# Performance work log

Measured on AMD Instinct MI355X. Metric: run time of the kernel, lower is better.

Reference implementation:

```python
import jax, jax.numpy as jnp
import numpy as np

B, T, H, W, C = 2, 4, 128, 128, 192
HEADS = 6
WS = 8          # attention window (per-frame, wsD=1)
OW = 12         # overlapping KV window: 8 + int(8*0.5)
PAD = (OW - WS) // 2
TBL = (WS + OW - 1) ** 2   # 361 relative-position-bias entries
MLP_HID = C * 2


def setup_inputs() -> dict:
    key = jax.random.key(0)
    ks = jax.random.split(key, 8)
    s = 0.02
    return dict(
        x=jax.random.normal(ks[0], (B, T, H, W, C), jnp.float32),
        x_size=jnp.array([H, W], jnp.int32),  # unused by forward (shadowed), kept for signature fidelity
        rpi_oca=jax.random.randint(ks[1], (WS * WS, OW * OW), 0, TBL),
        norm1_g=jnp.ones((C,), jnp.float32), norm1_b=jnp.zeros((C,), jnp.float32),
        qkv_w=jax.random.normal(ks[2], (C, 3 * C), jnp.float32) * s,
        qkv_b=jnp.zeros((3 * C,), jnp.float32),
        rpb_table=jax.random.normal(ks[3], (TBL, HEADS), jnp.float32) * s,
        norm2_g=jnp.ones((C,), jnp.float32), norm2_b=jnp.zeros((C,), jnp.float32),
        fc1_w=jax.random.normal(ks[4], (C, MLP_HID), jnp.float32) * s,
        fc1_b=jnp.zeros((MLP_HID,), jnp.float32),
        fc2_w=jax.random.normal(ks[5], (MLP_HID, C), jnp.float32) * s,
        fc2_b=jnp.zeros((C,), jnp.float32),
    )


def _ln(x, g, b):
    m = x.mean(-1, keepdims=True)
    v = ((x - m) ** 2).mean(-1, keepdims=True)
    return (x - m) * jax.lax.rsqrt(v + 1e-5) * g + b


def reference(x, x_size, rpi_oca, norm1_g, norm1_b, qkv_w, qkv_b, rpb_table,
              norm2_g, norm2_b, fc1_w, fc1_b, fc2_w, fc2_b):
    b, t, h, w, c = x.shape
    d = c // HEADS
    scale = d ** -0.5
    nH, nW = h // WS, w // WS
    b_ = b * t * nH * nW  # total windows
    shortcut = x
    xn = _ln(x, norm1_g, norm1_b)
    qkv = (xn @ qkv_w + qkv_b).reshape(b, t, h, w, 3, c)
    q, k, v = qkv[..., 0, :], qkv[..., 1, :], qkv[..., 2, :]
    # --- query: non-overlapping (1,8,8) windows -> (b_, heads, 64, d)
    qw = (q.reshape(b, t, nH, WS, nW, WS, c)
           .transpose(0, 1, 2, 4, 3, 5, 6)
           .reshape(b_, WS * WS, HEADS, d)
           .transpose(0, 2, 1, 3))
    # --- key/value: overlapping (1,12,12) windows with stride 8, zero-padded by 2
    hid = (jnp.arange(nH) * WS)[:, None] + jnp.arange(OW)  # (nH, OW)
    wid = (jnp.arange(nW) * WS)[:, None] + jnp.arange(OW)  # (nW, OW)

    def owin(z):
        zp = jnp.pad(z, ((0, 0), (0, 0), (PAD, PAD), (PAD, PAD), (0, 0)))
        zw = zp[:, :, hid][:, :, :, :, wid]  # (b, t, nH, OW, nW, OW, c)
        return (zw.transpose(0, 1, 2, 4, 3, 5, 6)
                  .reshape(b_, OW * OW, HEADS, d)
                  .transpose(0, 2, 1, 3))

    kw, vw = owin(k), owin(v)
    attn = jnp.einsum('bhqd,bhkd->bhqk', qw * scale, kw)  # (b_, heads, 64, 144)
    bias = rpb_table[rpi_oca.reshape(-1)].reshape(WS * WS, OW * OW, HEADS).transpose(2, 0, 1)
    attn = attn + bias[None]  # NOTE: original forward applies NO softmax (self.softmax unused)
    out = (jnp.einsum('bhqk,bhkd->bhqd', attn, vw)
             .transpose(0, 2, 1, 3)
             .reshape(b_, WS * WS, c))
    # window_reverse
    xa = (out.reshape(b, t, nH, nW, WS, WS, c)
             .transpose(0, 1, 2, 4, 3, 5, 6)
             .reshape(b, t, h, w, c))
    x = xa + shortcut  # self.proj is never applied in the original forward
    hmlp = jax.nn.gelu(_ln(x, norm2_g, norm2_b) @ fc1_w + fc1_b, approximate=False)
    return x + (hmlp @ fc2_w + fc2_b)
```

## Files before the change

### kernel.cpp

```cpp
#include <hip/hip_runtime.h>
#include <cstdint>
#include <cstddef>

typedef short bf16x8 __attribute__((ext_vector_type(8)));
typedef unsigned short u16x4 __attribute__((ext_vector_type(4)));
typedef float f32x4  __attribute__((ext_vector_type(4)));
typedef unsigned short u16;

#define DEVI __device__ __forceinline__

constexpr int C     = 192;
constexpr int HEADS = 6;
constexpr int NQKV  = 576;
constexpr int HID   = 384;
constexpr int NTOK  = 131072;

DEVI u16 f2bf(float f){
  union { float f; unsigned u; } v; v.f = f;
  return (u16)((v.u + 0x7fffu + ((v.u >> 16) & 1u)) >> 16);
}

DEVI float gelu(float xx){
  float y  = xx * 0.70710678118654752f;
  float ay = fabsf(y);
  float t  = __builtin_amdgcn_rcpf(1.0f + 0.3275911f * ay);
  float p  = t*(0.254829592f + t*(-0.284496736f + t*(1.421413741f + t*(-1.453152027f + t*1.061405429f))));
  float e  = __expf(-(y*y));
  float er = copysignf(1.0f - p*e, y);
  return 0.5f * xx * (1.0f + er);
}

__global__ void prep_kernel(const float* __restrict__ qkv_w,
                            const float* __restrict__ fc1_w,
                            const float* __restrict__ fc2_w,
                            const int*   __restrict__ rpi,
                            const float* __restrict__ rpb,
                            u16* __restrict__ qkvP,
                            u16* __restrict__ fc1P,
                            u16* __restrict__ fc2P,
                            float* __restrict__ bias_pk){
  int idx = blockIdx.x * blockDim.x + threadIdx.x;
  int stride = gridDim.x * blockDim.x;
  for(int i = idx; i < 36*6*64*8; i += stride){
    int e = i & 7, lane = (i >> 3) & 63, t = i >> 9;
    int ks = t % 6, p = t / 6;
    int n = p*16 + (lane & 15), k = ks*32 + (lane >> 4)*8 + e;
    qkvP[i] = f2bf(qkv_w[k*NQKV + n]);
  }
  for(int i = idx; i < 24*6*64*8; i += stride){
    int e = i & 7, lane = (i >> 3) & 63, t = i >> 9;
    int ks = t % 6, p = t / 6;
    int n = p*16 + (lane & 15), k = ks*32 + (lane >> 4)*8 + e;
    fc1P[i] = f2bf(fc1_w[k*HID + n]);
  }
  for(int i = idx; i < 12*12*64*8; i += stride){
    int e = i & 7, lane = (i >> 3) & 63, t = i >> 9;
    int ks = t % 12, p = t / 12;
    int n = p*16 + (lane & 15), k = ks*32 + (lane >> 4)*8 + e;
    fc2P[i] = f2bf(fc2_w[k*C + n]);
  }
  const int n4 = HEADS*5*2*4*64*4;
  for(int i = idx; i < n4; i += stride){
    int t = i;
    int r    = t & 3;  t >>= 2;
    int lane = t & 63; t >>= 6;
    int mi   = t & 3;  t >>= 2;
    int nf   = t & 1;  t >>= 1;
    int chunk = t % 5; int head = t / 5;
    int q  = mi*16 + (lane & 15);
    int kk = chunk*32 + nf*16 + ((lane >> 4) << 2) + r;
    float v = 0.f;
    if(kk < 144) v = rpb[rpi[q*144 + kk]*HEADS + head];
    bias_pk[i] = v;
  }
}

__global__ __launch_bounds__(384, 4)
void qkv_kernel(const float* __restrict__ x,
                const float* __restrict__ g1,
                const float* __restrict__ b1,
                const u16* __restrict__ wP,
                const float* __restrict__ qb,
                u16* __restrict__ qkv){
  __shared__ u16 xn[64][200];
  __shared__ u16 rp[64][152];
  const int tid = threadIdx.x;
  const int bid = blockIdx.x;
  const int nh = (bid >> 3) & 1;
  const int tb = (bid & 7) + ((bid >> 4) << 3);
  const size_t tok0 = (size_t)tb * 64;
  if(tid < 256){
    const int trow = tid >> 2;
    const int j = tid & 3;
    const float* xr = x + (tok0 + trow)*C;
    float4 xv[12];
    #pragma unroll
    for(int u = 0; u < 12; ++u)
      xv[u] = *reinterpret_cast<const float4*>(xr + u*16 + j*4);
    float s1 = 0.f, s2 = 0.f;
    #pragma unroll
    for(int u = 0; u < 12; ++u){
      const float* f = reinterpret_cast<const float*>(&xv[u]);
      #pragma unroll
      for(int e = 0; e < 4; ++e){ s1 += f[e]; s2 += f[e]*f[e]; }
    }
    s1 += __shfl_xor(s1, 1, 64); s2 += __shfl_xor(s2, 1, 64);
    s1 += __shfl_xor(s1, 2, 64); s2 += __shfl_xor(s2, 2, 64);
    const float mean = s1 * (1.f/192.f);
    const float rstd = rsqrtf(s2*(1.f/192.f) - mean*mean + 1e-5f);
    #pragma unroll
    for(int u = 0; u < 12; ++u){
      const float4 gv = *reinterpret_cast<const float4*>(g1 + u*16 + j*4);
      const float4 bv = *reinterpret_cast<const float4*>(b1 + u*16 + j*4);
      const float* f = reinterpret_cast<const float*>(&xv[u]);
      const float* gp = reinterpret_cast<const float*>(&gv);
      const float* bp = reinterpret_cast<const float*>(&bv);
      u16x4 pk;
      #pragma unroll
      for(int e = 0; e < 4; ++e) pk[e] = f2bf((f[e] - mean)*rstd*gp[e] + bp[e]);
      *reinterpret_cast<u16x4*>(&xn[trow][u*16 + j*4]) = pk;
    }
  }
  __syncthreads();
  const int lane = tid & 63;
  const int wn = tid >> 6;
  const int g = lane >> 4, col = lane & 15;
  const f32x4 fzero = {0.f, 0.f, 0.f, 0.f};
  f32x4 acc[4][3];
  #pragma unroll
  for(int mi = 0; mi < 4; ++mi)
    #pragma unroll
    for(int nf = 0; nf < 3; ++nf) acc[mi][nf] = fzero;
  const int p0 = nh*18 + wn*3;
  #pragma unroll
  for(int ks = 0; ks < 6; ++ks){
    bf16x8 wf[3];
    #pragma unroll
    for(int nf = 0; nf < 3; ++nf)
      wf[nf] = *reinterpret_cast<const bf16x8*>(wP + ((size_t)(((p0 + nf)*6 + ks)*64) + lane)*8);
    bf16x8 a[4];
    #pragma unroll
    for(int mi = 0; mi < 4; ++mi)
      a[mi] = *reinterpret_cast<const bf16x8*>(&xn[mi*16 + col][ks*32 + g*8]);
    #pragma unroll
    for(int nf = 0; nf < 3; ++nf)
      #pragma unroll
      for(int mi = 0; mi < 4; ++mi)
        acc[mi][nf] = __builtin_amdgcn_mfma_f32_16x16x32_bf16(a[mi], wf[nf], acc[mi][nf], 0, 0, 0);
  }
  #pragma unroll
  for(int ph = 0; ph < 2; ++ph){
    if(wn >= ph*3 && wn < ph*3 + 3){
      const int wl = wn - ph*3;
      #pragma unroll
      for(int mi = 0; mi < 4; ++mi){
        #pragma unroll
        for(int nf = 0; nf < 3; ++nf){
          const int nloc = wl*48 + nf*16 + col;
          const float bb = qb[nh*288 + ph*144 + nloc];
          #pragma unroll
          for(int r = 0; r < 4; ++r)
            rp[mi*16 + g*4 + r][nloc] = f2bf(acc[mi][nf][r] + bb);
        }
      }
    }
    __syncthreads();
    #pragma unroll
    for(int it = 0; it < 3; ++it){
      const int c = tid + it*384;
      const int tok = c / 18, cc = c - tok*18;
      const int n0 = nh*288 + ph*144 + cc*8;
      const int pl = n0 >> 5, d0 = n0 & 31;
      bf16x8 vv = *reinterpret_cast<const bf16x8*>(&rp[tok][cc*8]);
      *reinterpret_cast<bf16x8*>(qkv + ((size_t)pl*NTOK + tok0 + tok)*32 + d0) = vv;
    }
    __syncthreads();
  }
}

__global__ __launch_bounds__(64, 2)
void attn_kernel(const u16* __restrict__ qkv,
                 const float* __restrict__ bias_pk,
                 const float* __restrict__ x,
                 float* __restrict__ out){
  __shared__ u16 Vt[32][168];
  __shared__ u16 Pl[64][40];
  const int lane = threadIdx.x;
  const int g = lane >> 4, col = lane & 15;
  const int win = blockIdx.x, head = blockIdx.y;
  const int bt = win >> 8, wh = (win >> 4) & 15, ww = win & 15;
  const int h0 = wh*8, w0 = ww*8;
  const size_t tokbase = (size_t)bt * 16384;
  const u16* Qp = qkv + (size_t)head      *NTOK*32;
  const u16* Kp = qkv + (size_t)(6 + head)*NTOK*32;
  const u16* Vp = qkv + (size_t)(12 + head)*NTOK*32;
  const bf16x8 z8 = {0,0,0,0,0,0,0,0};

  bf16x8 kf[10], vf[10];
  #pragma unroll
  for(int i = 0; i < 10; ++i){
    const int kr = i*16 + col;
    const int r12 = (kr*2731) >> 15;
    const int c12 = kr - r12*12;
    const int hh = h0 - 2 + r12;
    const int wp = w0 - 2 + c12;
    const bool valid = (kr < 144) && (hh >= 0) && (hh < 128) && (wp >= 0) && (wp < 128);
    const size_t t = valid ? (tokbase + (size_t)hh*128 + wp) : tokbase;
    bf16x8 kv_ = *reinterpret_cast<const bf16x8*>(Kp + t*32 + g*8);
    bf16x8 vv_ = *reinterpret_cast<const bf16x8*>(Vp + t*32 + g*8);
    kf[i] = valid ? kv_ : z8;
    vf[i] = valid ? vv_ : z8;
  }
  bf16x8 qf[4];
  #pragma unroll
  for(int mi = 0; mi < 4; ++mi){
    const int row = mi*16 + col;
    const size_t t = tokbase + (size_t)(h0 + (row >> 3))*128 + (w0 + (row & 7));
    qf[mi] = *reinterpret_cast<const bf16x8*>(Qp + t*32 + g*8);
  }
  #pragma unroll
  for(int i = 0; i < 10; ++i) asm volatile("" : "+v"(kf[i]));
  #pragma unroll
  for(int mi = 0; mi < 4; ++mi) asm volatile("" : "+v"(qf[mi]));
  #pragma unroll
  for(int i = 0; i < 10; ++i){
    const int kr = i*16 + col;
    #pragma unroll
    for(int e = 0; e < 8; ++e) Vt[g*8 + e][kr] = (u16)vf[i][e];
  }

  const f32x4 fzero = {0.f, 0.f, 0.f, 0.f};
  f32x4 oacc[4][2];
  #pragma unroll
  for(int mi = 0; mi < 4; ++mi){ oacc[mi][0] = fzero; oacc[mi][1] = fzero; }
  const float scale = 0.17677669529663689f;

  #pragma unroll
  for(int ch = 0; ch < 5; ++ch){
    float4 bv[2][4];
    #pragma unroll
    for(int nf = 0; nf < 2; ++nf)
      #pragma unroll
      for(int mi = 0; mi < 4; ++mi)
        bv[nf][mi] = *reinterpret_cast<const float4*>(
            bias_pk + (size_t)((((head*5 + ch)*2 + nf)*4 + mi)*64 + lane)*4);
    f32x4 st[2][4];
    #pragma unroll
    for(int nf = 0; nf < 2; ++nf)
      #pragma unroll
      for(int mi = 0; mi < 4; ++mi)
        st[nf][mi] = __builtin_amdgcn_mfma_f32_16x16x32_bf16(kf[ch*2 + nf], qf[mi], fzero, 0, 0, 0);
    #pragma unroll
    for(int nf = 0; nf < 2; ++nf){
      #pragma unroll
      for(int mi = 0; mi < 4; ++mi){
        const float* bp = reinterpret_cast<const float*>(&bv[nf][mi]);
        const float p0 = fmaf(st[nf][mi][0], scale, bp[0]);
        const float p1 = fmaf(st[nf][mi][1], scale, bp[1]);
        const float p2 = fmaf(st[nf][mi][2], scale, bp[2]);
        const float p3 = fmaf(st[nf][mi][3], scale, bp[3]);
        uint2 pw;
        pw.x = (unsigned)f2bf(p0) | ((unsigned)f2bf(p1) << 16);
        pw.y = (unsigned)f2bf(p2) | ((unsigned)f2bf(p3) << 16);
        *reinterpret_cast<uint2*>(
            reinterpret_cast<char*>(&Pl[0][0]) + (mi*16 + col)*80 + nf*32 + g*8) = pw;
      }
    }
    bf16x8 pa[4];
    #pragma unroll
    for(int mi = 0; mi < 4; ++mi)
      pa[mi] = *reinterpret_cast<const bf16x8*>(
          reinterpret_cast<const char*>(&Pl[0][0]) + (mi*16 + col)*80 + g*16);
    bf16x8 vfr[2];
    #pragma unroll
    for(int nf = 0; nf < 2; ++nf)
      vfr[nf] = *reinterpret_cast<const bf16x8*>(&Vt[nf*16 + col][ch*32 + g*8]);
    #pragma unroll
    for(int nf = 0; nf < 2; ++nf)
      #pragma unroll
      for(int mi = 0; mi < 4; ++mi)
        oacc[mi][nf] = __builtin_amdgcn_mfma_f32_16x16x32_bf16(pa[mi], vfr[nf], oacc[mi][nf], 0, 0, 0);
  }
  #pragma unroll
  for(int mi = 0; mi < 4; ++mi){
    #pragma unroll
    for(int nf = 0; nf < 2; ++nf){
      #pragma unroll
      for(int r = 0; r < 4; ++r){
        const int row = mi*16 + g*4 + r;
        const int hh = h0 + (row >> 3), wp = w0 + (row & 7);
        const size_t o = (tokbase + hh*128 + wp)*(size_t)C + head*32 + nf*16 + col;
        out[o] = oacc[mi][nf][r] + x[o];
      }
    }
  }
}

__global__ __launch_bounds__(512, 4)
void mlp_kernel(float* __restrict__ io,
                const float* __restrict__ g2,
                const float* __restrict__ b2,
                const u16* __restrict__ w1P,
                const float* __restrict__ fb1,
                const u16* __restrict__ w2P,
                const float* __restrict__ fb2){
  __shared__ u16 xn[64][200];
  __shared__ u16 hl[64][200];
  const int tid = threadIdx.x;
  const size_t tok0 = (size_t)blockIdx.x * 64;
  {
    const int trow = tid >> 3;
    const int j = tid & 7;
    const float* xr = io + (tok0 + trow)*C;
    float4 xv[6];
    #pragma unroll
    for(int u = 0; u < 6; ++u)
      xv[u] = *reinterpret_cast<const float4*>(xr + u*32 + j*4);
    float s1 = 0.f, s2 = 0.f;
    #pragma unroll
    for(int u = 0; u < 6; ++u){
      const float* f = reinterpret_cast<const float*>(&xv[u]);
      #pragma unroll
      for(int e = 0; e < 4; ++e){ s1 += f[e]; s2 += f[e]*f[e]; }
    }
    s1 += __shfl_xor(s1, 1, 64); s2 += __shfl_xor(s2, 1, 64);
    s1 += __shfl_xor(s1, 2, 64); s2 += __shfl_xor(s2, 2, 64);
    s1 += __shfl_xor(s1, 4, 64); s2 += __shfl_xor(s2, 4, 64);
    const float mean = s1 * (1.f/192.f);
    const float rstd = rsqrtf(s2*(1.f/192.f) - mean*mean + 1e-5f);
    #pragma unroll
    for(int u = 0; u < 6; ++u){
      const float4 gv = *reinterpret_cast<const float4*>(g2 + u*32 + j*4);
      const float4 bv = *reinterpret_cast<const float4*>(b2 + u*32 + j*4);
      const float* f = reinterpret_cast<const float*>(&xv[u]);
      const float* gp = reinterpret_cast<const float*>(&gv);
      const float* bp = reinterpret_cast<const float*>(&bv);
      u16x4 pk;
      #pragma unroll
      for(int e = 0; e < 4; ++e) pk[e] = f2bf((f[e] - mean)*rstd*gp[e] + bp[e]);
      *reinterpret_cast<u16x4*>(&xn[trow][u*32 + j*4]) = pk;
    }
  }
  __syncthreads();
  const int lane = tid & 63, wave = tid >> 6;
  const int wm = wave >> 2;
  const int wn = wave & 3;
  const int g = lane >> 4, col = lane & 15;
  const f32x4 fzero = {0.f, 0.f, 0.f, 0.f};
  f32x4 acc2[2][3];
  #pragma unroll
  for(int mi = 0; mi < 2; ++mi)
    #pragma unroll
    for(int nf = 0; nf < 3; ++nf) acc2[mi][nf] = fzero;
  #pragma unroll
  for(int hb = 0; hb < 2; ++hb){
    f32x4 acc1[2][3];
    #pragma unroll
    for(int mi = 0; mi < 2; ++mi)
      #pragma unroll
      for(int nf = 0; nf < 3; ++nf) acc1[mi][nf] = fzero;
    #pragma unroll
    for(int ks = 0; ks < 6; ++ks){
      bf16x8 wf[3];
      #pragma unroll
      for(int nf = 0; nf < 3; ++nf)
        wf[nf] = *reinterpret_cast<const bf16x8*>(w1P + ((size_t)(((hb*12 + wn*3 + nf)*6 + ks)*64) + lane)*8);
      bf16x8 a[2];
      #pragma unroll
      for(int mi = 0; mi < 2; ++mi)
        a[mi] = *reinterpret_cast<const bf16x8*>(&xn[wm*32 + mi*16 + col][ks*32 + g*8]);
      #pragma unroll
      for(int nf = 0; nf < 3; ++nf)
        #pragma unroll
        for(int mi = 0; mi < 2; ++mi)
          acc1[mi][nf] = __builtin_amdgcn_mfma_f32_16x16x32_bf16(a[mi], wf[nf], acc1[mi][nf], 0, 0, 0);
    }
    #pragma unroll
    for(int mi = 0; mi < 2; ++mi){
      #pragma unroll
      for(int nf = 0; nf < 3; ++nf){
        const int nl = wn*48 + nf*16 + col;
        const float bb = fb1[hb*192 + nl];
        #pragma unroll
        for(int r = 0; r < 4; ++r){
          const int row = wm*32 + mi*16 + g*4 + r;
          hl[row][nl] = f2bf(gelu(acc1[mi][nf][r] + bb));
        }
      }
    }
    __syncthreads();
    #pragma unroll
    for(int ks = 0; ks < 6; ++ks){
      bf16x8 wf[3];
      #pragma unroll
      for(int nf = 0; nf < 3; ++nf)
        wf[nf] = *reinterpret_cast<const bf16x8*>(w2P + ((size_t)(((wn*3 + nf)*12 + hb*6 + ks)*64) + lane)*8);
      bf16x8 a[2];
      #pragma unroll
      for(int mi = 0; mi < 2; ++mi)
        a[mi] = *reinterpret_cast<const bf16x8*>(&hl[wm*32 + mi*16 + col][ks*32 + g*8]);
      #pragma unroll
      for(int nf = 0; nf < 3; ++nf)
        #pragma unroll
        for(int mi = 0; mi < 2; ++mi)
          acc2[mi][nf] = __builtin_amdgcn_mfma_f32_16x16x32_bf16(a[mi], wf[nf], acc2[mi][nf], 0, 0, 0);
    }
    __syncthreads();
  }
  #pragma unroll
  for(int mi = 0; mi < 2; ++mi){
    #pragma unroll
    for(int nf = 0; nf < 3; ++nf){
      const int n = wn*48 + nf*16 + col;
      const float bb = fb2[n];
      #pragma unroll
      for(int r = 0; r < 4; ++r){
        const int row = wm*32 + mi*16 + g*4 + r;
        const size_t idx = (tok0 + row)*C + n;
        io[idx] = acc2[mi][nf][r] + bb + io[idx];
      }
    }
  }
}

extern "C" void kernel_launch(void* const* d_in, const int* in_sizes, int n_in,
                              void* d_out, int out_size, void* d_ws, size_t ws_size,
                              hipStream_t stream){
  const float* x    = (const float*)d_in[0];
  const int*   rpi  = (const int*)  d_in[2];
  const float* n1g  = (const float*)d_in[3];
  const float* n1b  = (const float*)d_in[4];
  const float* qkvw = (const float*)d_in[5];
  const float* qkvb = (const float*)d_in[6];
  const float* rpb  = (const float*)d_in[7];
  const float* n2g  = (const float*)d_in[8];
  const float* n2b  = (const float*)d_in[9];
  const float* fc1w = (const float*)d_in[10];
  const float* fc1b = (const float*)d_in[11];
  const float* fc2w = (const float*)d_in[12];
  const float* fc2b = (const float*)d_in[13];
  float* out = (float*)d_out;
  char* ws = (char*)d_ws;
  u16*   qkvP    = (u16*)  (ws + 0);
  u16*   fc1P    = (u16*)  (ws + 221184);
  u16*   fc2P    = (u16*)  (ws + 368640);
  float* bias_pk = (float*)(ws + 516096);
  u16*   qkvbuf  = (u16*)  (ws + 1499136);
  if(ws_size < 152494080ull) return;
  prep_kernel<<<dim3(512), dim3(256), 0, stream>>>(qkvw, fc1w, fc2w, rpi, rpb, qkvP, fc1P, fc2P, bias_pk);
  qkv_kernel<<<dim3(4096), dim3(384), 0, stream>>>(x, n1g, n1b, qkvP, qkvb, qkvbuf);
  attn_kernel<<<dim3(2048, 6), dim3(64), 0, stream>>>(qkvbuf, bias_pk, x, out);
  mlp_kernel<<<dim3(2048), dim3(512), 0, stream>>>(out, n2g, n2b, fc1P, fc1b, fc2P, fc2b);
}
```

Baseline: 280.8 us.

## Split attention window across four waves sharing K/V through LDS

```diff
diff --git a/kernel.cpp b/kernel.cpp
--- a/kernel.cpp
+++ b/kernel.cpp
@@ -178,14 +178,17 @@
   }
 }
 
-__global__ __launch_bounds__(64, 2)
+__global__ __launch_bounds__(256, 4)
 void attn_kernel(const u16* __restrict__ qkv,
                  const float* __restrict__ bias_pk,
                  const float* __restrict__ x,
                  float* __restrict__ out){
+  __shared__ u16 Kl[160][40];
   __shared__ u16 Vt[32][168];
   __shared__ u16 Pl[64][40];
-  const int lane = threadIdx.x;
+  const int tid  = threadIdx.x;
+  const int lane = tid & 63;
+  const int w    = tid >> 6;
   const int g = lane >> 4, col = lane & 15;
   const int win = blockIdx.x, head = blockIdx.y;
   const int bt = win >> 8, wh = (win >> 4) & 15, ww = win & 15;
@@ -196,107 +199,90 @@
   const u16* Vp = qkv + (size_t)(12 + head)*NTOK*32;
   const bf16x8 z8 = {0,0,0,0,0,0,0,0};
 
-  bf16x8 kf[10], vf[10];
-  #pragma unroll
-  for(int i = 0; i < 10; ++i){
-    const int kr = i*16 + col;
-    const int r12 = (kr*2731) >> 15;
-    const int c12 = kr - r12*12;
-    const int hh = h0 - 2 + r12;
-    const int wp = w0 - 2 + c12;
-    const bool valid = (kr < 144) && (hh >= 0) && (hh < 128) && (wp >= 0) && (wp < 128);
-    const size_t t = valid ? (tokbase + (size_t)hh*128 + wp) : tokbase;
-    bf16x8 kv_ = *reinterpret_cast<const bf16x8*>(Kp + t*32 + g*8);
-    bf16x8 vv_ = *reinterpret_cast<const bf16x8*>(Vp + t*32 + g*8);
-    kf[i] = valid ? kv_ : z8;
-    vf[i] = valid ? vv_ : z8;
-  }
-  bf16x8 qf[4];
-  #pragma unroll
-  for(int mi = 0; mi < 4; ++mi){
-    const int row = mi*16 + col;
+  #pragma unroll
+  for(int ii = 0; ii < 3; ++ii){
+    const int i = w + ii*4;
+    if(i < 10){
+      const int kr = i*16 + col;
+      const int r12 = (kr*2731) >> 15;
+      const int c12 = kr - r12*12;
+      const int hh = h0 - 2 + r12;
+      const int wp = w0 - 2 + c12;
+      const bool valid = (kr < 144) && (hh >= 0) && (hh < 128) && (wp >= 0) && (wp < 128);
+      const size_t t = valid ? (tokbase + (size_t)hh*128 + wp) : tokbase;
+      bf16x8 kv_ = *reinterpret_cast<const bf16x8*>(Kp + t*32 + g*8);
+      bf16x8 vv_ = *reinterpret_cast<const bf16x8*>(Vp + t*32 + g*8);
+      kv_ = valid ? kv_ : z8;
+      vv_ = valid ? vv_ : z8;
+      *reinterpret_cast<bf16x8*>(&Kl[kr][g*8]) = kv_;
+      #pragma unroll
+      for(int e = 0; e < 8; ++e) Vt[g*8 + e][kr] = (u16)vv_[e];
+    }
+  }
+  bf16x8 qf;
+  {
+    const int row = w*16 + col;
     const size_t t = tokbase + (size_t)(h0 + (row >> 3))*128 + (w0 + (row & 7));
-    qf[mi] = *reinterpret_cast<const bf16x8*>(Qp + t*32 + g*8);
-  }
-  #pragma unroll
-  for(int i = 0; i < 10; ++i) asm volatile("" : "+v"(kf[i]));
-  #pragma unroll
-  for(int mi = 0; mi < 4; ++mi) asm volatile("" : "+v"(qf[mi]));
-  #pragma unroll
-  for(int i = 0; i < 10; ++i){
-    const int kr = i*16 + col;
-    #pragma unroll
-    for(int e = 0; e < 8; ++e) Vt[g*8 + e][kr] = (u16)vf[i][e];
-  }
+    qf = *reinterpret_cast<const bf16x8*>(Qp + t*32 + g*8);
+  }
+  __syncthreads();
 
   const f32x4 fzero = {0.f, 0.f, 0.f, 0.f};
-  f32x4 oacc[4][2];
-  #pragma unroll
-  for(int mi = 0; mi < 4; ++mi){ oacc[mi][0] = fzero; oacc[mi][1] = fzero; }
+  f32x4 oacc[2];
+  oacc[0] = fzero; oacc[1] = fzero;
   const float scale = 0.17677669529663689f;
 
   #pragma unroll
   for(int ch = 0; ch < 5; ++ch){
-    float4 bv[2][4];
+    float4 bv[2];
     #pragma unroll
     for(int nf = 0; nf < 2; ++nf)
-      #pragma unroll
-      for(int mi = 0; mi < 4; ++mi)
-        bv[nf][mi] = *reinterpret_cast<const float4*>(
-            bias_pk + (size_t)((((head*5 + ch)*2 + nf)*4 + mi)*64 + lane)*4);
-    f32x4 st[2][4];
+      bv[nf] = *reinterpret_cast<const float4*>(
+          bias_pk + (size_t)((((head*5 + ch)*2 + nf)*4 + w)*64 + lane)*4);
+    bf16x8 kfr[2];
     #pragma unroll
     for(int nf = 0; nf < 2; ++nf)
-      #pragma unroll
-      for(int mi = 0; mi < 4; ++mi)
-        st[nf][mi] = __builtin_amdgcn_mfma_f32_16x16x32_bf16(kf[ch*2 + nf], qf[mi], fzero, 0, 0, 0);
+      kfr[nf] = *reinterpret_cast<const bf16x8*>(&Kl[ch*32 + nf*16 + col][g*8]);
+    f32x4 st[2];
+    #pragma unroll
+    for(int nf = 0; nf < 2; ++nf)
+      st[nf] = __builtin_amdgcn_mfma_f32_16x16x32_bf16(kfr[nf], qf, fzero, 0, 0, 0);
     #pragma unroll
     for(int nf = 0; nf < 2; ++nf){
-      #pragma unroll
-      for(int mi = 0; mi < 4; ++mi){
-        const float* bp = reinterpret_cast<const float*>(&bv[nf][mi]);
-        const float p0 = fmaf(st[nf][mi][0], scale, bp[0]);
-        const float p1 = fmaf(st[nf][mi][1], scale, bp[1]);
-        const float p2 = fmaf(st[nf][mi][2], scale, bp[2]);
-        const float p3 = fmaf(st[nf][mi][3], scale, bp[3]);
-        uint2 pw;
-        pw.x = (unsigned)f2bf(p0) | ((unsigned)f2bf(p1) << 16);
-        pw.y = (unsigned)f2bf(p2) | ((unsigned)f2bf(p3) << 16);
-        *reinterpret_cast<uint2*>(
-            reinterpret_cast<char*>(&Pl[0][0]) + (mi*16 + col)*80 + nf*32 + g*8) = pw;
-      }
-    }
-    bf16x8 pa[4];
-    #pragma unroll
-    for(int mi = 0; mi < 4; ++mi)
-      pa[mi] = *reinterpret_cast<const bf16x8*>(
-          reinterpret_cast<const char*>(&Pl[0][0]) + (mi*16 + col)*80 + g*16);
+      const float* bp = reinterpret_cast<const float*>(&bv[nf]);
+      const float p0 = fmaf(st[nf][0], scale, bp[0]);
+      const float p1 = fmaf(st[nf][1], scale, bp[1]);
+      const float p2 = fmaf(st[nf][2], scale, bp[2]);
+      const float p3 = fmaf(st[nf][3], scale, bp[3]);
+      uint2 pw;
+      pw.x = (unsigned)f2bf(p0) | ((unsigned)f2bf(p1) << 16);
+      pw.y = (unsigned)f2bf(p2) | ((unsigned)f2bf(p3) << 16);
+      *reinterpret_cast<uint2*>(
+          reinterpret_cast<char*>(&Pl[0][0]) + (w*16 + col)*80 + nf*32 + g*8) = pw;
+    }
+    bf16x8 pa = *reinterpret_cast<const bf16x8*>(
+        reinterpret_cast<const char*>(&Pl[0][0]) + (w*16 + col)*80 + g*16);
     bf16x8 vfr[2];
     #pragma unroll
     for(int nf = 0; nf < 2; ++nf)
       vfr[nf] = *reinterpret_cast<const bf16x8*>(&Vt[nf*16 + col][ch*32 + g*8]);
     #pragma unroll
     for(int nf = 0; nf < 2; ++nf)
-      #pragma unroll
-      for(int mi = 0; mi < 4; ++mi)
-        oacc[mi][nf] = __builtin_amdgcn_mfma_f32_16x16x32_bf16(pa[mi], vfr[nf], oacc[mi][nf], 0, 0, 0);
-  }
-  #pragma unroll
-  for(int mi = 0; mi < 4; ++mi){
-    #pragma unroll
-    for(int nf = 0; nf < 2; ++nf){
-      #pragma unroll
-      for(int r = 0; r < 4; ++r){
-        const int row = mi*16 + g*4 + r;
-        const int hh = h0 + (row >> 3), wp = w0 + (row & 7);
-        const size_t o = (tokbase + hh*128 + wp)*(size_t)C + head*32 + nf*16 + col;
-        out[o] = oacc[mi][nf][r] + x[o];
-      }
-    }
-  }
-}
-
-__global__ __launch_bounds__(512, 4)
+      oacc[nf] = __builtin_amdgcn_mfma_f32_16x16x32_bf16(pa, vfr[nf], oacc[nf], 0, 0, 0);
+  }
+  #pragma unroll
+  for(int nf = 0; nf < 2; ++nf){
+    #pragma unroll
+    for(int r = 0; r < 4; ++r){
+      const int row = w*16 + g*4 + r;
+      const int hh = h0 + (row >> 3), wp = w0 + (row & 7);
+      const size_t o = (tokbase + hh*128 + wp)*(size_t)C + head*32 + nf*16 + col;
+      out[o] = oacc[nf][r] + x[o];
+    }
+  }
+}
+
+__global__ __launch_bounds__(512, 2)
 void mlp_kernel(float* __restrict__ io,
                 const float* __restrict__ g2,
                 const float* __restrict__ b2,
@@ -449,6 +435,6 @@
   if(ws_size < 152494080ull) return;
   prep_kernel<<<dim3(512), dim3(256), 0, stream>>>(qkvw, fc1w, fc2w, rpi, rpb, qkvP, fc1P, fc2P, bias_pk);
   qkv_kernel<<<dim3(4096), dim3(384), 0, stream>>>(x, n1g, n1b, qkvP, qkvb, qkvbuf);
-  attn_kernel<<<dim3(2048, 6), dim3(64), 0, stream>>>(qkvbuf, bias_pk, x, out);
+  attn_kernel<<<dim3(2048, 6), dim3(256), 0, stream>>>(qkvbuf, bias_pk, x, out);
   mlp_kernel<<<dim3(2048), dim3(512), 0, stream>>>(out, n2g, n2b, fc1P, fc1b, fc2P, fc2b);
 }
```

Result: no change. 281.9 us (+0.4%).
